# Optimization experiments

Hardware: AMD Instinct MI355X
Metric: run time of the kernel (lower is better)

The kernel has to match this reference:

```python
import jax, jax.numpy as jnp
import numpy as np

N_POINTS = 1 << 20
N_LEVELS = 16
F_PER_LVL = 2
LOG2_T = 19
T = 1 << LOG2_T
BASE_RES = 16
PER_LEVEL_SCALE = float(np.exp2(np.log2(2048.0 / 16.0) / (N_LEVELS - 1)))
# 8 trilinear corner offsets [8,3]
OFFSETS = np.stack(np.meshgrid(*([np.array([0, 1])] * 3), indexing='ij'), axis=-1).reshape(8, 3)
PRIMES = np.array([1, 2654435761, 805459861], dtype=np.uint32)  # tcnn spatial hash primes


def _level_params(l):
    # tcnn: grid_scale = 2^(l*log2(s)) * base - 1 ; resolution = ceil(scale)+1
    scale = np.exp2(l * np.log2(PER_LEVEL_SCALE)) * BASE_RES - 1.0
    res = int(np.ceil(scale)) + 1
    return float(scale), res


def hash_encode(x, table):
    """x: [N,3] in [0,1]; table: [L,T,F]. Returns [N, L*F]."""
    offs = jnp.asarray(OFFSETS)                     # [8,3] int32
    primes = jnp.asarray(PRIMES)                    # [3] uint32
    feats = []
    for l in range(N_LEVELS):
        scale, res = _level_params(l)
        pos = x * scale + 0.5                       # [N,3]
        pos_grid = jnp.floor(pos)
        w = pos - pos_grid                          # [N,3] interp weights
        c0 = pos_grid.astype(jnp.int32)             # [N,3]
        corners = c0[None, :, :] + offs[:, None, :]  # [8,N,3]
        if res ** 3 <= T:
            # dense indexing for coarse levels (fits in hashmap)
            cc = jnp.clip(corners, 0, res - 1)
            idx = cc[..., 0] + cc[..., 1] * res + cc[..., 2] * (res * res)
        else:
            cu = corners.astype(jnp.uint32)
            h = (cu[..., 0] * primes[0]) ^ (cu[..., 1] * primes[1]) ^ (cu[..., 2] * primes[2])
            idx = (h & jnp.uint32(T - 1)).astype(jnp.int32)
        f = table[l][idx]                           # [8,N,F] gather
        # trilinear weights: prod over dims of (w if corner bit else 1-w)
        wc = jnp.prod(jnp.where(offs[:, None, :] == 1, w[None], 1.0 - w[None]), axis=-1)  # [8,N]
        feats.append(jnp.sum(wc[..., None] * f, axis=0))  # [N,F]
    return jnp.concatenate(feats, axis=-1)          # [N, 32]


def _softplus10(z):
    return jax.nn.softplus(10.0 * z) / 10.0


def setup_inputs() -> dict:
    key = jax.random.key(0)
    k = jax.random.split(key, 6)
    x = jax.random.uniform(k[0], (N_POINTS, 3), dtype=jnp.float32)
    table = jax.random.normal(k[1], (N_LEVELS, T, F_PER_LVL), dtype=jnp.float32) * 1e-2
    w1 = jax.random.normal(k[2], (64, 32), dtype=jnp.float32) * 0.1
    w2 = jax.random.normal(k[3], (64, 64), dtype=jnp.float32) * 0.1
    w3 = jax.random.normal(k[4], (64, 64), dtype=jnp.float32) * 0.1
    w4 = jax.random.normal(k[5], (1, 64), dtype=jnp.float32) * 0.1
    return {"x": x, "table": table, "w1": w1, "w2": w2, "w3": w3, "w4": w4}


def reference(x, table, w1, w2, w3, w4):
    enc = hash_encode(x, table)                     # [N,32]
    h = _softplus10(enc @ w1.T)
    h = _softplus10(h @ w2.T)
    h = _softplus10(h @ w3.T)
    sdf = h @ w4.T                                  # [N,1]
    return sdf
```

## Files before the change

kernel.cpp:

```cpp
#include <hip/hip_runtime.h>
#include <cmath>

#define T_SIZE (1u << 19)
#define NBINS 32768

typedef _Float16 h8 __attribute__((ext_vector_type(8)));
typedef _Float16 h4 __attribute__((ext_vector_type(4)));
typedef _Float16 h2 __attribute__((ext_vector_type(2)));
typedef float f4 __attribute__((ext_vector_type(4)));

struct Levels {
    float scale[16];
    int   res[16];
    unsigned dense_mask;
};

__device__ __forceinline__ float softplus10(float z) {
    float e = __builtin_amdgcn_exp2f(fminf(z * 14.426950408889634f, 126.0f));
    return __builtin_amdgcn_logf(1.0f + e) * 0.069314718055994531f;
}

__global__ __launch_bounds__(256) void convert_kernel(
    const float2* __restrict__ t, h2* __restrict__ o, int total4,
    const float* __restrict__ w1, const float* __restrict__ w2,
    const float* __restrict__ w3, _Float16* __restrict__ wh)
{
    int i = blockIdx.x * 256 + threadIdx.x;
    if (i < total4) {
        const float2* src = t + (size_t)i * 4;
        h8 r;
#pragma unroll
        for (int j = 0; j < 4; ++j) {
            float2 v = src[j];
            r[2 * j]     = (_Float16)v.x;
            r[2 * j + 1] = (_Float16)v.y;
        }
        *(h8*)(o + (size_t)i * 4) = r;
    } else {
        int k = i - total4;
        if (k < 10240) {
            float v = (k < 2048) ? w1[k] : (k < 6144) ? w2[k - 2048] : w3[k - 6144];
            wh[k] = (_Float16)v;
        }
    }
}

__device__ __forceinline__ unsigned spread3(unsigned v) {
    v &= 1023u;
    v = (v | (v << 16)) & 0x030000FFu;
    v = (v | (v << 8))  & 0x0300F00Fu;
    v = (v | (v << 4))  & 0x030C30C3u;
    v = (v | (v << 2))  & 0x09249249u;
    return v;
}

__device__ __forceinline__ unsigned morton_key(float px, float py, float pz) {
    unsigned qx = (unsigned)fminf(fmaxf(px, 0.f) * 32.f, 31.f);
    unsigned qy = (unsigned)fminf(fmaxf(py, 0.f) * 32.f, 31.f);
    unsigned qz = (unsigned)fminf(fmaxf(pz, 0.f) * 32.f, 31.f);
    return (spread3(qx) << 2) | (spread3(qy) << 1) | spread3(qz);
}

__global__ __launch_bounds__(256) void zero_bins_kernel(unsigned* __restrict__ bins) {
    bins[blockIdx.x * 256 + threadIdx.x] = 0u;
}

__global__ __launch_bounds__(256) void hist_kernel(
    const float* __restrict__ xs, unsigned* __restrict__ bins, int N)
{
    int i = blockIdx.x * 256 + threadIdx.x;
    if (i >= N) return;
    unsigned k = morton_key(xs[3 * i], xs[3 * i + 1], xs[3 * i + 2]);
    atomicAdd(&bins[k], 1u);
}

__global__ __launch_bounds__(1024) void scan_kernel(
    const unsigned* __restrict__ bins, unsigned* __restrict__ cursor)
{
    __shared__ unsigned tmp[1024];
    const int t = threadIdx.x;
    unsigned loc[32];
    unsigned s = 0;
#pragma unroll
    for (int j = 0; j < 32; ++j) { loc[j] = s; s += bins[t * 32 + j]; }
    tmp[t] = s;
    __syncthreads();
    for (int d = 1; d < 1024; d <<= 1) {
        unsigned v = (t >= d) ? tmp[t - d] : 0u;
        __syncthreads();
        tmp[t] += v;
        __syncthreads();
    }
    unsigned base = (t > 0) ? tmp[t - 1] : 0u;
#pragma unroll
    for (int j = 0; j < 32; ++j) cursor[t * 32 + j] = base + loc[j];
}

__global__ __launch_bounds__(256) void scatter_kernel(
    const float* __restrict__ xs, float4* __restrict__ sx4,
    unsigned* __restrict__ cursor, int N)
{
    int i = blockIdx.x * 256 + threadIdx.x;
    if (i >= N) return;
    float px = xs[3 * i], py = xs[3 * i + 1], pz = xs[3 * i + 2];
    unsigned k = morton_key(px, py, pz);
    unsigned pos = atomicAdd(&cursor[k], 1u);
    sx4[pos] = make_float4(px, py, pz, __uint_as_float((unsigned)i));
}

__device__ __forceinline__ void gather_pair(
    const h2* __restrict__ tl, unsigned i0, unsigned i1,
    float2& v0, float2& v1)
{
    unsigned g = i0 & ~3u;
    union { h8 v; uint4 u; } cv;
    cv.v = *(const h8*)(tl + g);
    unsigned p0 = i0 & 3u;
    unsigned a01 = (p0 & 1u) ? cv.u.y : cv.u.x;
    unsigned a23 = (p0 & 1u) ? cv.u.w : cv.u.z;
    unsigned e0  = (p0 & 2u) ? a23 : a01;
    unsigned e1;
    if ((i1 & ~3u) == g) {
        unsigned p1 = i1 & 3u;
        unsigned b01 = (p1 & 1u) ? cv.u.y : cv.u.x;
        unsigned b23 = (p1 & 1u) ? cv.u.w : cv.u.z;
        e1 = (p1 & 2u) ? b23 : b01;
    } else {
        e1 = *(const unsigned*)(tl + i1);
    }
    h2 c0 = __builtin_bit_cast(h2, e0);
    h2 c1 = __builtin_bit_cast(h2, e1);
    v0 = make_float2((float)c0[0], (float)c0[1]);
    v1 = make_float2((float)c1[0], (float)c1[1]);
}

__device__ __forceinline__ h2 encode_point(
    float px, float py, float pz, float s, int res, bool dense,
    const h2* __restrict__ tl)
{
    float fx = px * s + 0.5f, fy = py * s + 0.5f, fz = pz * s + 0.5f;
    float gx = floorf(fx), gy = floorf(fy), gz = floorf(fz);
    float wx = fx - gx, wy = fy - gy, wz = fz - gz;
    int cx = (int)gx, cy = (int)gy, cz = (int)gz;

    float2 vx0[4], vx1[4];
    if (dense) {
        int r1 = res - 1;
        int x0 = min(cx, r1), x1 = min(cx + 1, r1);
        int y0 = min(cy, r1), y1 = min(cy + 1, r1);
        int z0 = min(cz, r1), z1 = min(cz + 1, r1);
        int rr = res * res;
        int bases[4] = {y0 * res + z0 * rr, y0 * res + z1 * rr,
                        y1 * res + z0 * rr, y1 * res + z1 * rr};
#pragma unroll
        for (int j = 0; j < 4; ++j)
            gather_pair(tl, (unsigned)(x0 + bases[j]), (unsigned)(x1 + bases[j]),
                        vx0[j], vx1[j]);
    } else {
        unsigned hy0 = (unsigned)cy * 2654435761u, hy1 = (unsigned)(cy + 1) * 2654435761u;
        unsigned hz0 = (unsigned)cz * 805459861u,  hz1 = (unsigned)(cz + 1) * 805459861u;
        unsigned Y[4] = {hy0 ^ hz0, hy0 ^ hz1, hy1 ^ hz0, hy1 ^ hz1};
        const unsigned M = T_SIZE - 1;
#pragma unroll
        for (int j = 0; j < 4; ++j)
            gather_pair(tl, ((unsigned)cx ^ Y[j]) & M,
                        ((unsigned)(cx + 1) ^ Y[j]) & M, vx0[j], vx1[j]);
    }

    float wx0 = 1.f - wx, wy0 = 1.f - wy, wz0 = 1.f - wz;
    float wyz[4] = {wy0 * wz0, wy0 * wz, wy * wz0, wy * wz};
    float f0 = 0.f, f1 = 0.f;
#pragma unroll
    for (int j = 0; j < 4; ++j) {
        float w0 = wx0 * wyz[j], w1 = wx * wyz[j];
        f0 += w0 * vx0[j].x + w1 * vx1[j].x;
        f1 += w0 * vx0[j].y + w1 * vx1[j].y;
    }
    h2 r; r[0] = (_Float16)f0; r[1] = (_Float16)f1;
    return r;
}

__global__ __launch_bounds__(256) void encode_kernel(
    const float* __restrict__ xs, const h2* __restrict__ table,
    h2* __restrict__ enc2, Levels lv, int lbase, int N)
{
    __shared__ float sx[768];
    const int i0 = blockIdx.x * 256;
    for (int t = threadIdx.x; t < 768; t += 256) sx[t] = xs[(size_t)i0 * 3 + t];
    __syncthreads();

    const int l = lbase + blockIdx.y;
    const int i = i0 + threadIdx.x;
    if (i >= N) return;
    h2 r = encode_point(sx[threadIdx.x * 3], sx[threadIdx.x * 3 + 1],
                        sx[threadIdx.x * 3 + 2], lv.scale[l], lv.res[l],
                        (lv.dense_mask >> l) & 1u, table + (size_t)l * T_SIZE);
    enc2[(size_t)l * N + i] = r;
}

__global__ __launch_bounds__(256) void encode_kernel_sorted(
    const float4* __restrict__ xs4, const h2* __restrict__ table,
    h2* __restrict__ enc2, Levels lv, int lbase, int N)
{
    const int i = blockIdx.x * 256 + threadIdx.x;
    if (i >= N) return;
    const int l = lbase + blockIdx.y;
    float4 q = xs4[i];
    h2 r = encode_point(q.x, q.y, q.z, lv.scale[l], lv.res[l],
                        (lv.dense_mask >> l) & 1u, table + (size_t)l * T_SIZE);
    enc2[(size_t)l * N + i] = r;
}

template <typename WT>
__device__ __forceinline__ h8 load_frag8(const WT* p) {
    if constexpr (sizeof(WT) == 2) {
        return *(const h8*)p;
    } else {
        h8 r;
#pragma unroll
        for (int j = 0; j < 8; ++j) r[j] = (_Float16)p[j];
        return r;
    }
}

template <typename WT, bool LOCAL, bool SORTED>
__global__ __launch_bounds__(256, 3) void fused_kernel(
    const float* __restrict__ xs, const float4* __restrict__ xs4,
    const h2* __restrict__ table16, const h2* __restrict__ enc2,
    const WT* __restrict__ w1, const WT* __restrict__ w2,
    const WT* __restrict__ w3, const float* __restrict__ w4,
    float* __restrict__ out, Levels lv, int N)
{
    constexpr int AR = 72;
    __shared__ __align__(16) char smem[4 * 9216];
    __shared__ float sx[768];

    const int tid  = threadIdx.x;
    const int wave = tid >> 6;
    const int lane = tid & 63;
    const int lrow = lane & 15;
    const int quad = lane >> 4;
    const int base = blockIdx.x * 256;
    char* wmem = smem + wave * 9216;
    const f4 zero = {0.f, 0.f, 0.f, 0.f};

    float px, py, pz;
    unsigned oi = 0;
    if constexpr (SORTED) {
        float4 q = xs4[base + tid];
        px = q.x; py = q.y; pz = q.z;
        oi = __float_as_uint(q.w);
    } else {
        for (int t = tid; t < 768; t += 256) sx[t] = xs[(size_t)base * 3 + t];
        __syncthreads();
        px = sx[tid * 3]; py = sx[tid * 3 + 1]; pz = sx[tid * 3 + 2];
    }
    const int p = tid & 63;

    if (LOCAL) {
#pragma unroll
        for (int l = 5; l < 15; ++l) {
            h2 v = enc2[(size_t)l * N + base + tid];
            *(h2*)(wmem + ((l >> 2) << 10) + (p << 4) + ((l & 3) << 2)) = v;
        }
        const int LMAP[6] = {0, 1, 2, 3, 4, 15};
#pragma unroll 2
        for (int s6 = 0; s6 < 6; ++s6) {
            const int l = LMAP[s6];
            h2 v = encode_point(px, py, pz, lv.scale[l], lv.res[l],
                                (lv.dense_mask >> l) & 1u,
                                table16 + (size_t)l * T_SIZE);
            *(h2*)(wmem + ((l >> 2) << 10) + (p << 4) + ((l & 3) << 2)) = v;
        }
    } else {
#pragma unroll
        for (int l = 0; l < 16; ++l) {
            h2 v = enc2[(size_t)l * N + base + tid];
            *(h2*)(wmem + ((l >> 2) << 10) + (p << 4) + ((l & 3) << 2)) = v;
        }
    }

    asm volatile("" ::: "memory");

    h8 aW1[4];
#pragma unroll
    for (int tm = 0; tm < 4; ++tm)
        aW1[tm] = load_frag8(w1 + (tm * 16 + lrow) * 32 + quad * 8);
    h8 aW2[4][2], aW3[4][2];
#pragma unroll
    for (int tm = 0; tm < 4; ++tm)
#pragma unroll
        for (int km = 0; km < 2; ++km) {
            aW2[tm][km] = load_frag8(w2 + (tm * 16 + lrow) * 64 + km * 32 + quad * 8);
            aW3[tm][km] = load_frag8(w3 + (tm * 16 + lrow) * 64 + km * 32 + quad * 8);
        }
    h4 w4q[4];
#pragma unroll
    for (int tm = 0; tm < 4; ++tm)
#pragma unroll
        for (int r = 0; r < 4; ++r) w4q[tm][r] = (_Float16)w4[tm * 16 + quad * 4 + r];

    h8 bin[4];
#pragma unroll
    for (int t = 0; t < 4; ++t)
        bin[t] = *(const h8*)(wmem + (quad << 10) + ((t * 16 + lrow) << 4));

    _Float16* wAct = (_Float16*)wmem;

#pragma unroll
    for (int t = 0; t < 4; ++t) {
        const int arow = (t * 16 + lrow) * AR;
#pragma unroll
        for (int tm = 0; tm < 4; ++tm) {
            f4 acc = __builtin_amdgcn_mfma_f32_16x16x32_f16(aW1[tm], bin[t], zero, 0, 0, 0);
            h4 pk;
#pragma unroll
            for (int r = 0; r < 4; ++r) pk[r] = (_Float16)softplus10(acc[r]);
            *(h4*)&wAct[arow + tm * 16 + quad * 4] = pk;
        }
    }

#pragma unroll
    for (int t = 0; t < 4; ++t) {
        const int arow = (t * 16 + lrow) * AR;
        h8 b0 = *(const h8*)&wAct[arow + quad * 8];
        h8 b1 = *(const h8*)&wAct[arow + 32 + quad * 8];
        f4 accs[4];
#pragma unroll
        for (int tm = 0; tm < 4; ++tm) {
            f4 acc = __builtin_amdgcn_mfma_f32_16x16x32_f16(aW2[tm][0], b0, zero, 0, 0, 0);
            acc     = __builtin_amdgcn_mfma_f32_16x16x32_f16(aW2[tm][1], b1, acc,  0, 0, 0);
            accs[tm] = acc;
        }
#pragma unroll
        for (int tm = 0; tm < 4; ++tm) {
            h4 pk;
#pragma unroll
            for (int r = 0; r < 4; ++r) pk[r] = (_Float16)softplus10(accs[tm][r]);
            *(h4*)&wAct[arow + tm * 16 + quad * 4] = pk;
        }
    }

#pragma unroll
    for (int t = 0; t < 4; ++t) {
        const int arow = (t * 16 + lrow) * AR;
        h8 b0 = *(const h8*)&wAct[arow + quad * 8];
        h8 b1 = *(const h8*)&wAct[arow + 32 + quad * 8];
        float sum = 0.f;
#pragma unroll
        for (int tm = 0; tm < 4; ++tm) {
            f4 acc = __builtin_amdgcn_mfma_f32_16x16x32_f16(aW3[tm][0], b0, zero, 0, 0, 0);
            acc     = __builtin_amdgcn_mfma_f32_16x16x32_f16(aW3[tm][1], b1, acc,  0, 0, 0);
#pragma unroll
            for (int r = 0; r < 4; ++r)
                sum += (float)w4q[tm][r] * softplus10(acc[r]);
        }
        sum += __shfl_xor(sum, 16, 64);
        sum += __shfl_xor(sum, 32, 64);
        if constexpr (SORTED) {
            unsigned t_oi = __shfl(oi, t * 16 + lrow, 64);
            if (quad == 0) out[t_oi] = sum;
        } else {
            if (quad == 0)
                out[base + wave * 64 + t * 16 + lrow] = sum;
        }
    }
}

__global__ __launch_bounds__(256) void encode_kernel_f32(
    const float* __restrict__ xs, const float2* __restrict__ table,
    h2* __restrict__ enc2, Levels lv, int N)
{
    const int i = blockIdx.x * 256 + threadIdx.x;
    const int l = blockIdx.y;
    if (i >= N) return;
    float px = xs[3 * i], py = xs[3 * i + 1], pz = xs[3 * i + 2];
    float s = lv.scale[l];
    int res = lv.res[l];
    float fx = px * s + 0.5f, fy = py * s + 0.5f, fz = pz * s + 0.5f;
    float gx = floorf(fx), gy = floorf(fy), gz = floorf(fz);
    float wx = fx - gx, wy = fy - gy, wz = fz - gz;
    int cx = (int)gx, cy = (int)gy, cz = (int)gz;
    unsigned idx[8];
    if ((lv.dense_mask >> l) & 1u) {
        int r1 = res - 1;
        int x0 = min(cx, r1), x1 = min(cx + 1, r1);
        int y0 = min(cy, r1), y1 = min(cy + 1, r1);
        int z0 = min(cz, r1), z1 = min(cz + 1, r1);
        int rr = res * res;
        idx[0] = x0 + y0 * res + z0 * rr; idx[1] = x0 + y0 * res + z1 * rr;
        idx[2] = x0 + y1 * res + z0 * rr; idx[3] = x0 + y1 * res + z1 * rr;
        idx[4] = x1 + y0 * res + z0 * rr; idx[5] = x1 + y0 * res + z1 * rr;
        idx[6] = x1 + y1 * res + z0 * rr; idx[7] = x1 + y1 * res + z1 * rr;
    } else {
        unsigned hx0 = (unsigned)cx, hx1 = (unsigned)(cx + 1);
        unsigned hy0 = (unsigned)cy * 2654435761u, hy1 = (unsigned)(cy + 1) * 2654435761u;
        unsigned hz0 = (unsigned)cz * 805459861u,  hz1 = (unsigned)(cz + 1) * 805459861u;
        idx[0] = (hx0^hy0^hz0) & (T_SIZE-1); idx[1] = (hx0^hy0^hz1) & (T_SIZE-1);
        idx[2] = (hx0^hy1^hz0) & (T_SIZE-1); idx[3] = (hx0^hy1^hz1) & (T_SIZE-1);
        idx[4] = (hx1^hy0^hz0) & (T_SIZE-1); idx[5] = (hx1^hy0^hz1) & (T_SIZE-1);
        idx[6] = (hx1^hy1^hz0) & (T_SIZE-1); idx[7] = (hx1^hy1^hz1) & (T_SIZE-1);
    }
    const float2* tl = table + (size_t)l * T_SIZE;
    float wx0 = 1.f - wx, wy0 = 1.f - wy, wz0 = 1.f - wz;
    float wcs[8] = {wx0*wy0*wz0, wx0*wy0*wz, wx0*wy*wz0, wx0*wy*wz,
                    wx*wy0*wz0,  wx*wy0*wz,  wx*wy*wz0,  wx*wy*wz};
    float f0 = 0.f, f1 = 0.f;
#pragma unroll
    for (int c = 0; c < 8; ++c) {
        float2 v = tl[idx[c]];
        f0 += wcs[c] * v.x; f1 += wcs[c] * v.y;
    }
    h2 r; r[0] = (_Float16)f0; r[1] = (_Float16)f1;
    enc2[(size_t)l * N + i] = r;
}

extern "C" void kernel_launch(void* const* d_in, const int* in_sizes, int n_in,
                              void* d_out, int out_size, void* d_ws, size_t ws_size,
                              hipStream_t stream) {
    const float* x     = (const float*)d_in[0];
    const float* table = (const float*)d_in[1];
    const float* w1    = (const float*)d_in[2];
    const float* w2    = (const float*)d_in[3];
    const float* w3    = (const float*)d_in[4];
    const float* w4    = (const float*)d_in[5];
    float* out = (float*)d_out;
    const int N = in_sizes[0] / 3;

    Levels lv;
    lv.dense_mask = 0;
    const double pls = exp2(log2(2048.0 / 16.0) / 15.0);
    const double lg  = log2(pls);
    for (int l = 0; l < 16; ++l) {
        double sc = exp2((double)l * lg) * 16.0 - 1.0;
        int res = (int)ceil(sc) + 1;
        lv.scale[l] = (float)sc;
        lv.res[l]   = res;
        if ((long long)res * res * res <= (long long)T_SIZE) lv.dense_mask |= (1u << l);
    }

    const size_t encBytes   = (size_t)16 * N * 4;
    const size_t tableBytes = (size_t)16 * T_SIZE * 4;
    const size_t whBytes    = 32768;
    const size_t sx4Bytes   = (size_t)N * 16;
    const size_t binBytes   = (size_t)NBINS * 4 * 2;
    h2* enc2 = (h2*)d_ws;

    const int ptBlocks = (N + 255) / 256;

    if (ws_size >= encBytes + tableBytes + whBytes + sx4Bytes + binBytes) {
        h2* table16    = (h2*)((char*)d_ws + encBytes);
        _Float16* wh   = (_Float16*)((char*)d_ws + encBytes + tableBytes);
        float4* sx4    = (float4*)((char*)d_ws + encBytes + tableBytes + whBytes);
        unsigned* bins = (unsigned*)((char*)d_ws + encBytes + tableBytes + whBytes + sx4Bytes);
        unsigned* curs = bins + NBINS;

        const int total4 = 16 * T_SIZE / 4;
        const int convBlocks = (total4 + 10240 + 255) / 256;
        hipLaunchKernelGGL(convert_kernel, dim3(convBlocks), dim3(256), 0, stream,
                           (const float2*)table, table16, total4, w1, w2, w3, wh);

        hipLaunchKernelGGL(zero_bins_kernel, dim3(NBINS / 256), dim3(256), 0, stream, bins);
        hipLaunchKernelGGL(hist_kernel, dim3(ptBlocks), dim3(256), 0, stream, x, bins, N);
        hipLaunchKernelGGL(scan_kernel, dim3(1), dim3(1024), 0, stream, bins, curs);
        hipLaunchKernelGGL(scatter_kernel, dim3(ptBlocks), dim3(256), 0, stream,
                           x, sx4, curs, N);

        hipLaunchKernelGGL(encode_kernel_sorted, dim3(ptBlocks, 10), dim3(256), 0, stream,
                           (const float4*)sx4, (const h2*)table16, enc2, lv, 5, N);
        hipLaunchKernelGGL((fused_kernel<_Float16, true, true>), dim3(ptBlocks), dim3(256),
                           0, stream, x, (const float4*)sx4, (const h2*)table16,
                           (const h2*)enc2, wh, wh + 2048, wh + 6144, w4, out, lv, N);
    } else if (ws_size >= encBytes + tableBytes + whBytes) {
        h2* table16 = (h2*)((char*)d_ws + encBytes);
        _Float16* wh = (_Float16*)((char*)d_ws + encBytes + tableBytes);
        const int total4 = 16 * T_SIZE / 4;
        const int convBlocks = (total4 + 10240 + 255) / 256;
        hipLaunchKernelGGL(convert_kernel, dim3(convBlocks), dim3(256), 0, stream,
                           (const float2*)table, table16, total4, w1, w2, w3, wh);
        hipLaunchKernelGGL(encode_kernel, dim3(ptBlocks, 10), dim3(256), 0, stream,
                           x, (const h2*)table16, enc2, lv, 5, N);
        hipLaunchKernelGGL((fused_kernel<_Float16, true, false>), dim3(ptBlocks), dim3(256),
                           0, stream, x, (const float4*)nullptr, (const h2*)table16,
                           (const h2*)enc2, wh, wh + 2048, wh + 6144, w4, out, lv, N);
    } else {
        hipLaunchKernelGGL(encode_kernel_f32, dim3(ptBlocks, 16), dim3(256), 0, stream,
                           x, (const float2*)table, enc2, lv, N);
        hipLaunchKernelGGL((fused_kernel<float, false, false>), dim3(ptBlocks), dim3(256),
                           0, stream, x, (const float4*)nullptr, (const h2*)nullptr,
                           (const h2*)enc2, w1, w2, w3, w4, out, lv, N);
    }
}
```

Before: 491.8 us.

## Replace global-atomic Morton counting sort with two-pass block-local radix sort

```diff
diff --git a/kernel.cpp b/kernel.cpp
--- a/kernel.cpp
+++ b/kernel.cpp
@@ -2,7 +2,9 @@
 #include <cmath>
 
 #define T_SIZE (1u << 19)
-#define NBINS 32768
+#define CB 512
+#define NBLK 128
+#define RCAP 3584
 
 typedef _Float16 h8 __attribute__((ext_vector_type(8)));
 typedef _Float16 h4 __attribute__((ext_vector_type(4)));
@@ -61,28 +63,31 @@
     return (spread3(qx) << 2) | (spread3(qy) << 1) | spread3(qz);
 }
 
-__global__ __launch_bounds__(256) void zero_bins_kernel(unsigned* __restrict__ bins) {
-    bins[blockIdx.x * 256 + threadIdx.x] = 0u;
-}
-
 __global__ __launch_bounds__(256) void hist_kernel(
-    const float* __restrict__ xs, unsigned* __restrict__ bins, int N)
-{
-    int i = blockIdx.x * 256 + threadIdx.x;
-    if (i >= N) return;
-    unsigned k = morton_key(xs[3 * i], xs[3 * i + 1], xs[3 * i + 2]);
-    atomicAdd(&bins[k], 1u);
+    const float* __restrict__ xs, unsigned* __restrict__ M, int N)
+{
+    __shared__ unsigned h[CB];
+    for (int t = threadIdx.x; t < CB; t += 256) h[t] = 0u;
+    __syncthreads();
+    const int per = N / NBLK;
+    const int s = blockIdx.x * per;
+    for (int i = s + threadIdx.x; i < s + per; i += 256) {
+        unsigned k = morton_key(xs[3 * i], xs[3 * i + 1], xs[3 * i + 2]) >> 6;
+        atomicAdd(&h[k], 1u);
+    }
+    __syncthreads();
+    for (int t = threadIdx.x; t < CB; t += 256)
+        M[t * NBLK + blockIdx.x] = h[t];
 }
 
 __global__ __launch_bounds__(1024) void scan_kernel(
-    const unsigned* __restrict__ bins, unsigned* __restrict__ cursor)
+    const unsigned* __restrict__ M, unsigned* __restrict__ Ms)
 {
     __shared__ unsigned tmp[1024];
     const int t = threadIdx.x;
-    unsigned loc[32];
+    const int PER = (CB * NBLK) / 1024;
     unsigned s = 0;
-#pragma unroll
-    for (int j = 0; j < 32; ++j) { loc[j] = s; s += bins[t * 32 + j]; }
+    for (int j = 0; j < PER; ++j) s += M[t * PER + j];
     tmp[t] = s;
     __syncthreads();
     for (int d = 1; d < 1024; d <<= 1) {
@@ -91,21 +96,64 @@
         tmp[t] += v;
         __syncthreads();
     }
-    unsigned base = (t > 0) ? tmp[t - 1] : 0u;
-#pragma unroll
-    for (int j = 0; j < 32; ++j) cursor[t * 32 + j] = base + loc[j];
-}
-
-__global__ __launch_bounds__(256) void scatter_kernel(
-    const float* __restrict__ xs, float4* __restrict__ sx4,
-    unsigned* __restrict__ cursor, int N)
-{
-    int i = blockIdx.x * 256 + threadIdx.x;
-    if (i >= N) return;
-    float px = xs[3 * i], py = xs[3 * i + 1], pz = xs[3 * i + 2];
-    unsigned k = morton_key(px, py, pz);
-    unsigned pos = atomicAdd(&cursor[k], 1u);
-    sx4[pos] = make_float4(px, py, pz, __uint_as_float((unsigned)i));
+    unsigned run = (t > 0) ? tmp[t - 1] : 0u;
+    for (int j = 0; j < PER; ++j) {
+        unsigned v = M[t * PER + j];
+        Ms[t * PER + j] = run;
+        run += v;
+    }
+}
+
+__global__ __launch_bounds__(256) void cscatter_kernel(
+    const float* __restrict__ xs, const unsigned* __restrict__ Ms,
+    float4* __restrict__ sx4, int N)
+{
+    __shared__ unsigned cur[CB];
+    for (int t = threadIdx.x; t < CB; t += 256)
+        cur[t] = Ms[t * NBLK + blockIdx.x];
+    __syncthreads();
+    const int per = N / NBLK;
+    const int s = blockIdx.x * per;
+    for (int i = s + threadIdx.x; i < s + per; i += 256) {
+        float px = xs[3 * i], py = xs[3 * i + 1], pz = xs[3 * i + 2];
+        unsigned k = morton_key(px, py, pz) >> 6;
+        unsigned pos = atomicAdd(&cur[k], 1u);
+        sx4[pos] = make_float4(px, py, pz, __uint_as_float((unsigned)i));
+    }
+}
+
+__global__ __launch_bounds__(256) void refine_kernel(
+    float4* __restrict__ sx4, const unsigned* __restrict__ Ms, int N)
+{
+    __shared__ float4 pts[RCAP];
+    __shared__ unsigned h[64], base[64];
+    const int b = blockIdx.x;
+    const unsigned s = Ms[b * NBLK];
+    const unsigned e = (b == CB - 1) ? (unsigned)N : Ms[(b + 1) * NBLK];
+    const unsigned cnt = e - s;
+    if (cnt > RCAP) return;
+    if (threadIdx.x < 64) h[threadIdx.x] = 0u;
+    __syncthreads();
+    for (unsigned i = threadIdx.x; i < cnt; i += 256) {
+        float4 q = sx4[s + i];
+        pts[i] = q;
+        unsigned k = morton_key(q.x, q.y, q.z) & 63u;
+        atomicAdd(&h[k], 1u);
+    }
+    __syncthreads();
+    if (threadIdx.x == 0) {
+        unsigned a = 0;
+        for (int j = 0; j < 64; ++j) { base[j] = a; a += h[j]; }
+    }
+    __syncthreads();
+    if (threadIdx.x < 64) h[threadIdx.x] = 0u;
+    __syncthreads();
+    for (unsigned i = threadIdx.x; i < cnt; i += 256) {
+        float4 q = pts[i];
+        unsigned k = morton_key(q.x, q.y, q.z) & 63u;
+        unsigned r = base[k] + atomicAdd(&h[k], 1u);
+        sx4[s + r] = q;
+    }
 }
 
 __device__ __forceinline__ void gather_pair(
@@ -443,28 +491,30 @@
     const size_t tableBytes = (size_t)16 * T_SIZE * 4;
     const size_t whBytes    = 32768;
     const size_t sx4Bytes   = (size_t)N * 16;
-    const size_t binBytes   = (size_t)NBINS * 4 * 2;
+    const size_t mBytes     = (size_t)CB * NBLK * 4;
     h2* enc2 = (h2*)d_ws;
 
     const int ptBlocks = (N + 255) / 256;
 
-    if (ws_size >= encBytes + tableBytes + whBytes + sx4Bytes + binBytes) {
+    if (ws_size >= encBytes + tableBytes + whBytes + sx4Bytes + 2 * mBytes
+        && (N % NBLK) == 0) {
         h2* table16    = (h2*)((char*)d_ws + encBytes);
         _Float16* wh   = (_Float16*)((char*)d_ws + encBytes + tableBytes);
         float4* sx4    = (float4*)((char*)d_ws + encBytes + tableBytes + whBytes);
-        unsigned* bins = (unsigned*)((char*)d_ws + encBytes + tableBytes + whBytes + sx4Bytes);
-        unsigned* curs = bins + NBINS;
+        unsigned* M    = (unsigned*)((char*)d_ws + encBytes + tableBytes + whBytes + sx4Bytes);
+        unsigned* Ms   = M + (size_t)CB * NBLK;
 
         const int total4 = 16 * T_SIZE / 4;
         const int convBlocks = (total4 + 10240 + 255) / 256;
         hipLaunchKernelGGL(convert_kernel, dim3(convBlocks), dim3(256), 0, stream,
                            (const float2*)table, table16, total4, w1, w2, w3, wh);
 
-        hipLaunchKernelGGL(zero_bins_kernel, dim3(NBINS / 256), dim3(256), 0, stream, bins);
-        hipLaunchKernelGGL(hist_kernel, dim3(ptBlocks), dim3(256), 0, stream, x, bins, N);
-        hipLaunchKernelGGL(scan_kernel, dim3(1), dim3(1024), 0, stream, bins, curs);
-        hipLaunchKernelGGL(scatter_kernel, dim3(ptBlocks), dim3(256), 0, stream,
-                           x, sx4, curs, N);
+        hipLaunchKernelGGL(hist_kernel, dim3(NBLK), dim3(256), 0, stream, x, M, N);
+        hipLaunchKernelGGL(scan_kernel, dim3(1), dim3(1024), 0, stream, M, Ms);
+        hipLaunchKernelGGL(cscatter_kernel, dim3(NBLK), dim3(256), 0, stream,
+                           x, Ms, sx4, N);
+        hipLaunchKernelGGL(refine_kernel, dim3(CB), dim3(256), 0, stream,
+                           sx4, Ms, N);
 
         hipLaunchKernelGGL(encode_kernel_sorted, dim3(ptBlocks, 10), dim3(256), 0, stream,
                            (const float4*)sx4, (const h2*)table16, enc2, lv, 5, N);
```

Result: faster. 451.6 us (-8.2%).
